# Optimization experiments

Hardware: AMD Instinct MI355X
Metric: run time of the kernel (lower is better)

The kernel has to match this reference:

```python
import jax, jax.numpy as jnp
import numpy as np

N, F, EX, E = 50000, 128, 64, 500000
HID = 256
NEG_SLOPE = 0.01  # torch nn.LeakyReLU default
# (atom1 table, atom2 table) per branch; tables: 0=s,1=p,2=d,3=S
PAIRS = [(0,0),(0,1),(1,1),(1,1),(0,2),(1,2),(1,2),(2,2),(2,2),(2,2),(3,3),(3,0),(3,1),(3,2)]
D_IN = 2*F + EX  # 320


def setup_inputs() -> dict:
    key = jax.random.key(0)
    ks = jax.random.split(key, 12)
    inp = {
        'sfeat': jax.random.normal(ks[0], (N, F), jnp.float32),
        'pfeat': jax.random.normal(ks[1], (N, F), jnp.float32),
        'dfeat': jax.random.normal(ks[2], (N, F), jnp.float32),
        'Sfeat': jax.random.normal(ks[3], (N, F), jnp.float32),
        'hopping_index': jax.random.randint(ks[4], (E, 2), 0, N, jnp.int64),
        'd': jax.random.uniform(ks[5], (E, 1), jnp.float32, 1.0, 5.0),
        'ex_d': jax.random.normal(ks[6], (E, EX), jnp.float32),
        # 14 parallel 2-layer MLPs, stacked on leading branch axis
        'W1': jax.random.normal(ks[7], (14, D_IN, HID), jnp.float32) * 0.02,
        'b1': jnp.zeros((14, HID), jnp.float32),
        'W2': jax.random.normal(ks[8], (14, HID, 1), jnp.float32) * 0.02,
        'b2': jnp.zeros((14, 1), jnp.float32),
    }
    return inp


def reference(sfeat, pfeat, dfeat, Sfeat, W1, b1, W2, b2, hopping_index, d, ex_d):
    feats = (sfeat, pfeat, dfeat, Sfeat)
    atom1 = hopping_index[:, 0]
    atom2 = hopping_index[:, 1]
    d2 = d * d  # [E,1]
    outs = []
    for k, (i, j) in enumerate(PAIRS):
        # per-edge gather, divide by d^2, concat with ex_d -> [E, 2F+EX]
        x = jnp.concatenate([feats[i][atom1] / d2, feats[j][atom2] / d2, ex_d], axis=1)
        h = jax.nn.leaky_relu(x @ W1[k] + b1[k], NEG_SLOPE)
        outs.append(h @ W2[k] + b2[k])  # [E,1]
    return jnp.concatenate(outs, axis=-1)  # [E,14]
```

## Files before the change

### kernel.cpp

```cpp
#include <hip/hip_runtime.h>

#define NEDGE  500000
#define NTILE  7813
#define NCH    280
#define CHUNK  28
#define NPAIR  14

typedef _Float16 v8h __attribute__((ext_vector_type(8)));
typedef _Float16 v4h __attribute__((ext_vector_type(4)));
typedef float    v4f __attribute__((ext_vector_type(4)));

__constant__ int cI[14] = {0,0,1,1,0,1,1,2,2,2,3,3,3,3};
__constant__ int cJ[14] = {0,1,1,1,2,2,2,2,2,2,3,0,1,2};

__global__ __launch_bounds__(256) void prep_w1(const float* __restrict__ W1,
                                               _Float16* __restrict__ W1T) {
    int tid = blockIdx.x * 256 + threadIdx.x;
    if (tid >= 14*320*256) return;
    int n   = tid & 255;
    int t   = tid >> 8;
    int kk  = t % 320;
    int k14 = t / 320;
    float v = W1[tid];
    int dst = ((((k14*16 + (n>>4))*10 + (kk>>5))*4 + ((kk>>3)&3))*16 + (n&15))*8 + (kk&7);
    W1T[dst] = (_Float16)v;
}

__global__ __launch_bounds__(512, 2) void hopping_ws(
    const float* __restrict__ sfeat, const float* __restrict__ pfeat,
    const float* __restrict__ dfeat, const float* __restrict__ Sfeat,
    const int*  __restrict__ hop,   const float* __restrict__ darr,
    const float* __restrict__ exd,  const float* __restrict__ b1,
    const float* __restrict__ W2,   const float* __restrict__ b2,
    const _Float16* __restrict__ W1T, float* __restrict__ out)
{
    extern __shared__ char smem[];
    _Float16* xb0  = (_Float16*)smem;
    float*    part = (float*)(smem + 81920);

    const int tid = threadIdx.x;
    const int bid = blockIdx.x;

    const int xcd   = bid & 7;
    const int q     = bid >> 3;
    const int k14   = q % 14;
    const int chunk = xcd*35 + q/14;
    const long t0   = (long)chunk * CHUNK;
    int my_n = CHUNK;
    if (t0 + my_n > NTILE) my_n = (int)(NTILE - t0);

    const int i4 = cI[k14], j4 = cJ[k14];
    const float* gt = (i4==0)?sfeat:(i4==1)?pfeat:(i4==2)?dfeat:Sfeat;
    const float* ht = (j4==0)?sfeat:(j4==1)?pfeat:(j4==2)?dfeat:Sfeat;

    const int lane = tid & 63;
    const int w    = tid >> 6;
    const int col  = lane & 15;
    const int quad = lane >> 4;
    const int ser  = tid >> 3;
    const int sq   = tid & 7;

    v8h bfr[2][10];
    {
        const _Float16* wb = W1T + (size_t)k14 * 81920;
        #pragma unroll
        for (int nt = 0; nt < 2; ++nt)
            #pragma unroll
            for (int kc = 0; kc < 10; ++kc)
                bfr[nt][kc] = *(const v8h*)&wb[(((size_t)(w*2+nt)*10 + kc)*64 + lane)*8];
    }
    float b1v[2], w2v[2];
    #pragma unroll
    for (int nt = 0; nt < 2; ++nt) {
        int n = (w*2+nt)*16 + col;
        b1v[nt] = b1[k14*256 + n];
        w2v[nt] = W2[k14*256 + n];
    }
    const float b2v = b2[k14];

    float4 sg[4], sh[4], sx[2]; float sinv = 0.f;

    auto hopload = [&](int ti, int& a1, int& a2, float& dv) {
        long eg = (t0 + ti)*64 + ser; if (eg >= NEDGE) eg = NEDGE - 1;
        a1 = hop[2*eg]; a2 = hop[2*eg + 1]; dv = darr[eg];
    };
    auto gather_issue = [&](int ti, int a1, int a2, float dv) {
        sinv = 1.0f / (dv * dv);
        const float4* s1 = (const float4*)gt + (size_t)a1 * 32;
        const float4* s2 = (const float4*)ht + (size_t)a2 * 32;
        #pragma unroll
        for (int r = 0; r < 4; ++r) { sg[r] = s1[r*8 + sq]; sh[r] = s2[r*8 + sq]; }
        long eg = (t0 + ti)*64 + ser; if (eg >= NEDGE) eg = NEDGE - 1;
        const float4* s3 = (const float4*)exd + eg * 16;
        sx[0] = s3[sq]; sx[1] = s3[8 + sq];
    };
    auto stage_write = [&](_Float16* dst) {
        #pragma unroll
        for (int r = 0; r < 4; ++r) {
            int c  = r*8 + sq;
            int ch = c >> 1;
            int sz1 = (ch & ~7) | ((ch ^ ser) & 7);
            v4h hv; hv[0]=(_Float16)(sg[r].x*sinv); hv[1]=(_Float16)(sg[r].y*sinv);
                    hv[2]=(_Float16)(sg[r].z*sinv); hv[3]=(_Float16)(sg[r].w*sinv);
            *(v4h*)&dst[ser*320 + sz1*8 + (c&1)*4] = hv;
            int ch2 = 16 + ch;
            int sz2 = (ch2 & ~7) | ((ch2 ^ ser) & 7);
            v4h hu; hu[0]=(_Float16)(sh[r].x*sinv); hu[1]=(_Float16)(sh[r].y*sinv);
                    hu[2]=(_Float16)(sh[r].z*sinv); hu[3]=(_Float16)(sh[r].w*sinv);
            *(v4h*)&dst[ser*320 + sz2*8 + (c&1)*4] = hu;
        }
        #pragma unroll
        for (int r = 0; r < 2; ++r) {
            int c  = r*8 + sq;
            int ch = 32 + (c >> 1);
            int sz = (ch & ~7) | ((ch ^ ser) & 7);
            v4h hv; hv[0]=(_Float16)sx[r].x; hv[1]=(_Float16)sx[r].y;
                    hv[2]=(_Float16)sx[r].z; hv[3]=(_Float16)sx[r].w;
            *(v4h*)&dst[ser*320 + sz*8 + (c&1)*4] = hv;
        }
    };

    int ca1, ca2; float cdv;
    int fa1, fa2; float fdv;
    {
        int a1, a2; float dv;
        hopload(0, a1, a2, dv);
        gather_issue(0, a1, a2, dv);
        hopload(1, ca1, ca2, cdv);
        stage_write(xb0);
    }
    __syncthreads();

    #pragma unroll 1
    for (int ti = 0; ti < my_n; ++ti) {
        const int  cur = ti & 1;
        const bool hn  = (ti + 1 < my_n);

        if (hn)              gather_issue(ti+1, ca1, ca2, cdv);
        if (ti + 2 < my_n)   hopload(ti+2, fa1, fa2, fdv);

        const _Float16* xb = xb0 + cur*20480;
        v4f acc[4][2];
        #pragma unroll
        for (int a = 0; a < 4; ++a) {
            acc[a][0] = (v4f){0.f,0.f,0.f,0.f};
            acc[a][1] = (v4f){0.f,0.f,0.f,0.f};
        }
        #pragma unroll
        for (int kc = 0; kc < 10; ++kc) {
            v8h af[4];
            #pragma unroll
            for (int mt = 0; mt < 4; ++mt) {
                int row = mt*16 + col;
                int ck  = kc*4 + quad;
                int sz  = (ck & ~7) | ((ck ^ row) & 7);
                af[mt] = *(const v8h*)&xb[row*320 + sz*8];
            }
            #pragma unroll
            for (int mt = 0; mt < 4; ++mt)
                #pragma unroll
                for (int nt = 0; nt < 2; ++nt)
                    acc[mt][nt] = __builtin_amdgcn_mfma_f32_16x16x32_f16(
                        af[mt], bfr[nt][kc], acc[mt][nt], 0, 0, 0);
        }

        {
            float* pb = part + cur*8192;
            #pragma unroll
            for (int mt = 0; mt < 4; ++mt) {
                v4f pv = (v4f){0.f,0.f,0.f,0.f};
                #pragma unroll
                for (int nt = 0; nt < 2; ++nt)
                    #pragma unroll
                    for (int r = 0; r < 4; ++r) {
                        float hv = acc[mt][nt][r] + b1v[nt];
                        hv = (hv > 0.f) ? hv : 0.01f * hv;
                        pv[r] += hv * w2v[nt];
                    }
                int P  = w*16 + col;
                int Qx = (mt*4 + quad) ^ (col & 7) ^ w;
                *(v4f*)&pb[P*64 + Qx*4] = pv;
            }
        }

        if (hn) stage_write(xb0 + (cur^1)*20480);

        __syncthreads();

        {
            const float* pr = part + cur*8192;
            int row = tid >> 3, seg = tid & 7;
            int Q = row >> 2, r = row & 3;
            float v = 0.f;
            #pragma unroll
            for (int i = 0; i < 16; ++i) {
                int P  = seg*16 + i;
                int Qx = Q ^ (i & 7) ^ seg;
                v += pr[P*64 + Qx*4 + r];
            }
            v += __shfl_xor(v, 1, 8);
            v += __shfl_xor(v, 2, 8);
            v += __shfl_xor(v, 4, 8);
            if (seg == 0) {
                long eg = (t0 + ti)*64 + row;
                if (eg < NEDGE) out[eg*14 + k14] = v + b2v;
            }
        }

        ca1 = fa1; ca2 = fa2; cdv = fdv;
    }
}

extern "C" void kernel_launch(void* const* d_in, const int* in_sizes, int n_in,
                              void* d_out, int out_size, void* d_ws, size_t ws_size,
                              hipStream_t stream)
{
    (void)in_sizes; (void)n_in; (void)out_size; (void)ws_size;
    const float* sfeat = (const float*)d_in[0];
    const float* pfeat = (const float*)d_in[1];
    const float* dfeat = (const float*)d_in[2];
    const float* Sfeat = (const float*)d_in[3];
    const int*   hop   = (const int*)  d_in[4];
    const float* darr  = (const float*)d_in[5];
    const float* exd   = (const float*)d_in[6];
    const float* W1    = (const float*)d_in[7];
    const float* b1    = (const float*)d_in[8];
    const float* W2    = (const float*)d_in[9];
    const float* b2    = (const float*)d_in[10];
    _Float16* W1T = (_Float16*)d_ws;

    static bool attr_done = false;
    if (!attr_done) {
        hipFuncSetAttribute((const void*)hopping_ws,
                            hipFuncAttributeMaxDynamicSharedMemorySize, 147456);
        attr_done = true;
    }

    prep_w1<<<dim3(4480), dim3(256), 0, stream>>>(W1, W1T);

    hopping_ws<<<dim3(NCH * NPAIR), dim3(512), 147456, stream>>>(
        sfeat, pfeat, dfeat, Sfeat, hop, darr, exd, b1, W2, b2, W1T, (float*)d_out);
}
```

Baseline: 1.539 ms.

## Retile waves to 2x4 MFMA grid and split gather staging across K halves

```diff
diff --git a/kernel.cpp b/kernel.cpp
--- a/kernel.cpp
+++ b/kernel.cpp
@@ -7,7 +7,6 @@
 #define NPAIR  14
 
 typedef _Float16 v8h __attribute__((ext_vector_type(8)));
-typedef _Float16 v4h __attribute__((ext_vector_type(4)));
 typedef float    v4f __attribute__((ext_vector_type(4)));
 
 __constant__ int cI[14] = {0,0,1,1,0,1,1,2,2,2,3,3,3,3};
@@ -55,79 +54,101 @@
 
     const int lane = tid & 63;
     const int w    = tid >> 6;
+    const int wm   = w >> 2;
+    const int wn   = w & 3;
     const int col  = lane & 15;
     const int quad = lane >> 4;
     const int ser  = tid >> 3;
     const int sq   = tid & 7;
 
-    v8h bfr[2][10];
+    v8h bfr[4][10];
     {
         const _Float16* wb = W1T + (size_t)k14 * 81920;
         #pragma unroll
-        for (int nt = 0; nt < 2; ++nt)
+        for (int nt = 0; nt < 4; ++nt)
             #pragma unroll
             for (int kc = 0; kc < 10; ++kc)
-                bfr[nt][kc] = *(const v8h*)&wb[(((size_t)(w*2+nt)*10 + kc)*64 + lane)*8];
-    }
-    float b1v[2], w2v[2];
+                bfr[nt][kc] = *(const v8h*)&wb[(((size_t)(wn*4+nt)*10 + kc)*64 + lane)*8];
+    }
+    float b1v[4], w2v[4];
     #pragma unroll
-    for (int nt = 0; nt < 2; ++nt) {
-        int n = (w*2+nt)*16 + col;
+    for (int nt = 0; nt < 4; ++nt) {
+        int n = (wn*4+nt)*16 + col;
         b1v[nt] = b1[k14*256 + n];
         w2v[nt] = W2[k14*256 + n];
     }
     const float b2v = b2[k14];
 
     float4 sg[4], sh[4], sx[2]; float sinv = 0.f;
+    int ca1, ca2; float cdv;
+    int fa1, fa2; float fdv;
 
     auto hopload = [&](int ti, int& a1, int& a2, float& dv) {
         long eg = (t0 + ti)*64 + ser; if (eg >= NEDGE) eg = NEDGE - 1;
         a1 = hop[2*eg]; a2 = hop[2*eg + 1]; dv = darr[eg];
     };
-    auto gather_issue = [&](int ti, int a1, int a2, float dv) {
+    auto issue_gx = [&](int ti, int a1, float dv) {
         sinv = 1.0f / (dv * dv);
         const float4* s1 = (const float4*)gt + (size_t)a1 * 32;
-        const float4* s2 = (const float4*)ht + (size_t)a2 * 32;
-        #pragma unroll
-        for (int r = 0; r < 4; ++r) { sg[r] = s1[r*8 + sq]; sh[r] = s2[r*8 + sq]; }
+        #pragma unroll
+        for (int r = 0; r < 4; ++r) sg[r] = s1[sq*4 + r];
         long eg = (t0 + ti)*64 + ser; if (eg >= NEDGE) eg = NEDGE - 1;
         const float4* s3 = (const float4*)exd + eg * 16;
-        sx[0] = s3[sq]; sx[1] = s3[8 + sq];
-    };
-    auto stage_write = [&](_Float16* dst) {
-        #pragma unroll
-        for (int r = 0; r < 4; ++r) {
-            int c  = r*8 + sq;
-            int ch = c >> 1;
-            int sz1 = (ch & ~7) | ((ch ^ ser) & 7);
-            v4h hv; hv[0]=(_Float16)(sg[r].x*sinv); hv[1]=(_Float16)(sg[r].y*sinv);
-                    hv[2]=(_Float16)(sg[r].z*sinv); hv[3]=(_Float16)(sg[r].w*sinv);
-            *(v4h*)&dst[ser*320 + sz1*8 + (c&1)*4] = hv;
-            int ch2 = 16 + ch;
-            int sz2 = (ch2 & ~7) | ((ch2 ^ ser) & 7);
-            v4h hu; hu[0]=(_Float16)(sh[r].x*sinv); hu[1]=(_Float16)(sh[r].y*sinv);
-                    hu[2]=(_Float16)(sh[r].z*sinv); hu[3]=(_Float16)(sh[r].w*sinv);
-            *(v4h*)&dst[ser*320 + sz2*8 + (c&1)*4] = hu;
-        }
-        #pragma unroll
-        for (int r = 0; r < 2; ++r) {
-            int c  = r*8 + sq;
-            int ch = 32 + (c >> 1);
+        sx[0] = s3[sq*2]; sx[1] = s3[sq*2 + 1];
+    };
+    auto issue_h = [&](int a2) {
+        const float4* s2 = (const float4*)ht + (size_t)a2 * 32;
+        #pragma unroll
+        for (int r = 0; r < 4; ++r) sh[r] = s2[sq*4 + r];
+    };
+    auto write_gx = [&](_Float16* dst) {
+        #pragma unroll
+        for (int hf = 0; hf < 2; ++hf) {
+            float4 a = sg[hf*2], b = sg[hf*2+1];
+            v8h hv;
+            hv[0]=(_Float16)(a.x*sinv); hv[1]=(_Float16)(a.y*sinv);
+            hv[2]=(_Float16)(a.z*sinv); hv[3]=(_Float16)(a.w*sinv);
+            hv[4]=(_Float16)(b.x*sinv); hv[5]=(_Float16)(b.y*sinv);
+            hv[6]=(_Float16)(b.z*sinv); hv[7]=(_Float16)(b.w*sinv);
+            int ch = sq*2 + hf;
             int sz = (ch & ~7) | ((ch ^ ser) & 7);
-            v4h hv; hv[0]=(_Float16)sx[r].x; hv[1]=(_Float16)sx[r].y;
-                    hv[2]=(_Float16)sx[r].z; hv[3]=(_Float16)sx[r].w;
-            *(v4h*)&dst[ser*320 + sz*8 + (c&1)*4] = hv;
-        }
-    };
-
-    int ca1, ca2; float cdv;
-    int fa1, fa2; float fdv;
+            *(v8h*)&dst[ser*320 + sz*8] = hv;
+        }
+        {
+            float4 a = sx[0], b = sx[1];
+            v8h hv;
+            hv[0]=(_Float16)a.x; hv[1]=(_Float16)a.y;
+            hv[2]=(_Float16)a.z; hv[3]=(_Float16)a.w;
+            hv[4]=(_Float16)b.x; hv[5]=(_Float16)b.y;
+            hv[6]=(_Float16)b.z; hv[7]=(_Float16)b.w;
+            int ch = 32 + sq;
+            int sz = (ch & ~7) | ((ch ^ ser) & 7);
+            *(v8h*)&dst[ser*320 + sz*8] = hv;
+        }
+    };
+    auto write_h = [&](_Float16* dst) {
+        #pragma unroll
+        for (int hf = 0; hf < 2; ++hf) {
+            float4 a = sh[hf*2], b = sh[hf*2+1];
+            v8h hv;
+            hv[0]=(_Float16)(a.x*sinv); hv[1]=(_Float16)(a.y*sinv);
+            hv[2]=(_Float16)(a.z*sinv); hv[3]=(_Float16)(a.w*sinv);
+            hv[4]=(_Float16)(b.x*sinv); hv[5]=(_Float16)(b.y*sinv);
+            hv[6]=(_Float16)(b.z*sinv); hv[7]=(_Float16)(b.w*sinv);
+            int ch = 16 + sq*2 + hf;
+            int sz = (ch & ~7) | ((ch ^ ser) & 7);
+            *(v8h*)&dst[ser*320 + sz*8] = hv;
+        }
+    };
+
     {
         int a1, a2; float dv;
         hopload(0, a1, a2, dv);
-        gather_issue(0, a1, a2, dv);
+        issue_gx(0, a1, dv);
+        issue_h(a2);
         hopload(1, ca1, ca2, cdv);
-        stage_write(xb0);
+        write_gx(xb0);
+        write_h(xb0);
     }
     __syncthreads();
 
@@ -135,74 +156,97 @@
     for (int ti = 0; ti < my_n; ++ti) {
         const int  cur = ti & 1;
         const bool hn  = (ti + 1 < my_n);
-
-        if (hn)              gather_issue(ti+1, ca1, ca2, cdv);
+        const _Float16* xb  = xb0 + cur*20480;
+        _Float16*       nxt = xb0 + (cur^1)*20480;
+
+        if (hn)              issue_gx(ti+1, ca1, cdv);
         if (ti + 2 < my_n)   hopload(ti+2, fa1, fa2, fdv);
 
-        const _Float16* xb = xb0 + cur*20480;
-        v4f acc[4][2];
-        #pragma unroll
-        for (int a = 0; a < 4; ++a) {
-            acc[a][0] = (v4f){0.f,0.f,0.f,0.f};
-            acc[a][1] = (v4f){0.f,0.f,0.f,0.f};
-        }
-        #pragma unroll
-        for (int kc = 0; kc < 10; ++kc) {
-            v8h af[4];
-            #pragma unroll
-            for (int mt = 0; mt < 4; ++mt) {
-                int row = mt*16 + col;
+        v4f acc[2][4];
+        #pragma unroll
+        for (int a = 0; a < 2; ++a)
+            #pragma unroll
+            for (int b = 0; b < 4; ++b)
+                acc[a][b] = (v4f){0.f,0.f,0.f,0.f};
+
+        #pragma unroll
+        for (int kc = 0; kc < 5; ++kc) {
+            v8h af[2];
+            #pragma unroll
+            for (int mt = 0; mt < 2; ++mt) {
+                int row = wm*32 + mt*16 + col;
                 int ck  = kc*4 + quad;
                 int sz  = (ck & ~7) | ((ck ^ row) & 7);
                 af[mt] = *(const v8h*)&xb[row*320 + sz*8];
             }
             #pragma unroll
-            for (int mt = 0; mt < 4; ++mt)
+            for (int mt = 0; mt < 2; ++mt)
                 #pragma unroll
-                for (int nt = 0; nt < 2; ++nt)
+                for (int nt = 0; nt < 4; ++nt)
                     acc[mt][nt] = __builtin_amdgcn_mfma_f32_16x16x32_f16(
                         af[mt], bfr[nt][kc], acc[mt][nt], 0, 0, 0);
         }
 
+        if (hn) { write_gx(nxt); issue_h(ca2); }
+
+        #pragma unroll
+        for (int kc = 5; kc < 10; ++kc) {
+            v8h af[2];
+            #pragma unroll
+            for (int mt = 0; mt < 2; ++mt) {
+                int row = wm*32 + mt*16 + col;
+                int ck  = kc*4 + quad;
+                int sz  = (ck & ~7) | ((ck ^ row) & 7);
+                af[mt] = *(const v8h*)&xb[row*320 + sz*8];
+            }
+            #pragma unroll
+            for (int mt = 0; mt < 2; ++mt)
+                #pragma unroll
+                for (int nt = 0; nt < 4; ++nt)
+                    acc[mt][nt] = __builtin_amdgcn_mfma_f32_16x16x32_f16(
+                        af[mt], bfr[nt][kc], acc[mt][nt], 0, 0, 0);
+        }
+
         {
-            float* pb = part + cur*8192;
-            #pragma unroll
-            for (int mt = 0; mt < 4; ++mt) {
+            float* pb = part + cur*4096;
+            #pragma unroll
+            for (int mt = 0; mt < 2; ++mt) {
                 v4f pv = (v4f){0.f,0.f,0.f,0.f};
                 #pragma unroll
-                for (int nt = 0; nt < 2; ++nt)
+                for (int nt = 0; nt < 4; ++nt)
                     #pragma unroll
                     for (int r = 0; r < 4; ++r) {
                         float hv = acc[mt][nt][r] + b1v[nt];
                         hv = (hv > 0.f) ? hv : 0.01f * hv;
                         pv[r] += hv * w2v[nt];
                     }
-                int P  = w*16 + col;
-                int Qx = (mt*4 + quad) ^ (col & 7) ^ w;
+                int P  = wn*16 + col;
+                int Q  = wm*8 + mt*4 + quad;
+                int Qx = Q ^ col;
                 *(v4f*)&pb[P*64 + Qx*4] = pv;
             }
         }
 
-        if (hn) stage_write(xb0 + (cur^1)*20480);
+        if (hn) write_h(nxt);
 
         __syncthreads();
 
         {
-            const float* pr = part + cur*8192;
-            int row = tid >> 3, seg = tid & 7;
-            int Q = row >> 2, r = row & 3;
+            const float* pr = part + cur*4096;
+            int erow = tid >> 3, seg = tid & 7;
+            int Q = erow >> 2, r = erow & 3;
             float v = 0.f;
             #pragma unroll
-            for (int i = 0; i < 16; ++i) {
-                int P  = seg*16 + i;
-                int Qx = Q ^ (i & 7) ^ seg;
+            for (int i = 0; i < 8; ++i) {
+                int P  = (i << 3) | seg;
+                int Qx = Q ^ (P & 15);
                 v += pr[P*64 + Qx*4 + r];
             }
             v += __shfl_xor(v, 1, 8);
             v += __shfl_xor(v, 2, 8);
             v += __shfl_xor(v, 4, 8);
             if (seg == 0) {
-                long eg = (t0 + ti)*64 + row;
+                long eg = (t0 + ti)*64 + erow;
                 if (eg < NEDGE) out[eg*14 + k14] = v + b2v;
             }
         }
@@ -232,12 +276,12 @@
     static bool attr_done = false;
     if (!attr_done) {
         hipFuncSetAttribute((const void*)hopping_ws,
-                            hipFuncAttributeMaxDynamicSharedMemorySize, 147456);
+                            hipFuncAttributeMaxDynamicSharedMemorySize, 114688);
         attr_done = true;
     }
 
     prep_w1<<<dim3(4480), dim3(256), 0, stream>>>(W1, W1T);
 
-    hopping_ws<<<dim3(NCH * NPAIR), dim3(512), 147456, stream>>>(
+    hopping_ws<<<dim3(NCH * NPAIR), dim3(512), 114688, stream>>>(
         sfeat, pfeat, dfeat, Sfeat, hop, darr, exd, b1, W2, b2, W1T, (float*)d_out);
 }
```

New measurement: 5.183 ms. 237% more time.
